# Optimization experiments

Hardware: AMD Instinct MI355X
Metric: run time of the kernel (lower is better)

## Reference

```python
import jax, jax.numpy as jnp
import numpy as np

B, C, T = 8, 256, 2048
K = 10                     # n_neigh_seq
TEMPORAL_SCALE = 2048
SHORT_RATIO = 0.4
STITCH_GAP = 20


def setup_inputs() -> dict:
    key = jax.random.key(0)
    k1, k2, k3, k4 = jax.random.split(key, 4)
    x = jax.random.normal(k1, (B, C, T), dtype=jnp.float32)
    num_frms = jax.random.randint(k2, (B,), 0, 2048, dtype=jnp.int64 if jax.config.jax_enable_x64 else jnp.int32)
    W_conv = jax.random.normal(k3, (C, C, 3), dtype=jnp.float32) * 0.02  # Conv1d(out,in,k)
    b_conv = jnp.zeros((C,), dtype=jnp.float32)
    W_mlp = jax.random.normal(k4, (C, 2 * C), dtype=jnp.float32) * 0.02  # Linear(2C -> C)
    b_mlp = jnp.zeros((C,), dtype=jnp.float32)
    return {"x": x, "num_frms": num_frms, "W_conv": W_conv, "b_conv": b_conv,
            "W_mlp": W_mlp, "b_mlp": b_mlp}


def knn_neigh_idx(x, num_frms, k=K):
    """Vectorized translation of knn() + get_neigh_idx_semantic()."""
    b, c, t = x.shape
    ratio = TEMPORAL_SCALE / t
    half1 = k // 2
    half2 = k - half1
    # pairwise squared distances via ||xi||^2 + ||xj||^2 - 2 xi.xj (same math,
    # avoids the B*C*T*T intermediate the torch code materializes)
    sq = jnp.sum(x * x, axis=1)                           # [B,T]
    gram = jnp.einsum('bci,bcj->bij', x, x)               # [B,T,T]
    dif = sq[:, :, None] + sq[:, None, :] - 2.0 * gram    # [B,T,T]
    _, idx_org = jax.lax.top_k(-dif, k)                   # smallest-k -> [B,T,k]
    big = jnp.max(dif) + 1.0
    # per-batch short-video rewiring (original does a python loop over batch)
    cond = num_frms.astype(jnp.float32) <= SHORT_RATIO * TEMPORAL_SCALE   # [B]
    thr = (num_frms.astype(jnp.float32) + STITCH_GAP) / ratio             # [B]
    pos = jnp.arange(t)
    region = (pos[None, :, None] >= thr[:, None, None]) & \
             (pos[None, None, :] >= thr[:, None, None])                   # [B,T,T]
    dif_m = jnp.where(region, big, dif)
    # kill the already-chosen first half of neighbors, then re-topk the rest
    b_idx = jnp.arange(b)[:, None, None]
    r_idx = pos[None, :, None]
    dif_m = dif_m.at[b_idx, r_idx, idx_org[:, :, :half1]].set(big)
    _, idx2 = jax.lax.top_k(-dif_m, half2)                # [B,T,half2]
    tail = jnp.where(cond[:, None, None], idx2, idx_org[:, :, half1:])
    idx_new = jnp.concatenate([idx_org[:, :, :half1], tail], axis=-1)     # [B,T,k]
    shift = (jnp.arange(b) * t)[:, None, None]
    return (idx_new + shift).reshape(-1)                  # [B*T*k] flat node ids


def reference(x, num_frms, W_conv, b_conv, W_mlp, b_mlp):
    b, c, t = x.shape
    # tconv1: Conv1d k=3, s=1, p=1
    c_out = jax.lax.conv_general_dilated(
        x, W_conv, window_strides=(1,), padding=[(1, 1)],
        dimension_numbers=('NCH', 'OIH', 'NCH')) + b_conv[None, :, None]   # [B,C,T]
    # NeighConv on raw x (gcn_insert == 'par'), nfeat_mode='feat_ctr', agg='max'
    neigh = knn_neigh_idx(x, num_frms)                    # [B*T*K]
    feat = jnp.transpose(x, (0, 2, 1)).reshape(-1, c)     # [B*T, C]
    feat_neigh = feat[neigh].reshape(-1, K, c)            # [B*T, K, C]
    ctr = jnp.broadcast_to(feat[:, None, :], feat_neigh.shape)
    cat = jnp.concatenate([feat_neigh, ctr], axis=-1)     # [B*T, K, 2C]
    g = jnp.einsum('nkd,od->nko', cat, W_mlp) + b_mlp     # [B*T, K, C]
    g = jnp.max(g, axis=1)                                # max aggregation
    g_out = jnp.transpose(g.reshape(b, t, -1), (0, 2, 1)) # [B,C,T]
    out = jax.nn.relu(c_out + g_out)
    # MaxPool1d(kernel=2, stride=2)
    out = out.reshape(b, out.shape[1], t // 2, 2).max(axis=-1)
    return out
```

## Files before the change

### kernel.cpp

```cpp
#include <hip/hip_runtime.h>
#include <hip/hip_bf16.h>
#include <math.h>
#include <float.h>

#define NC 256
#define NT 2048

typedef __attribute__((ext_vector_type(4))) float f32x4;
typedef __attribute__((ext_vector_type(8))) short short8;
typedef __attribute__((ext_vector_type(8))) unsigned short ushort8;

#define SQ_OFF 0
#define A_OFF  131072
#define XL_OFF 8388608
#define E_OFF  16908288
#define NB_OFF 33685504

__device__ __forceinline__ int load_nf(const int* __restrict__ nf, int b) {
    bool is64 = (nf[1] == 0) & (nf[3] == 0) & (nf[5] == 0) & (nf[7] == 0);
    return is64 ? nf[2 * b] : nf[b];
}

__device__ __forceinline__ void split_bf16(float f, unsigned short& h, unsigned short& l) {
    __hip_bfloat16 hb = __float2bfloat16(f);
    float fh = __bfloat162float(hb);
    __hip_bfloat16 lb = __float2bfloat16(f - fh);
    h = *(unsigned short*)&hb;
    l = *(unsigned short*)&lb;
}

__device__ __forceinline__ float rl_f(float v, int srclane) {
    return __int_as_float(__builtin_amdgcn_readlane(__float_as_int(v), srclane));
}
__device__ __forceinline__ int rl_i(int v, int srclane) {
    return __builtin_amdgcn_readlane(v, srclane);
}
__device__ __forceinline__ float dpp_shr1_f(float v) {
    return __int_as_float(__builtin_amdgcn_update_dpp(0, __float_as_int(v), 0x111, 0xf, 0xf, false));
}
__device__ __forceinline__ int dpp_shr1_i(int v) {
    return __builtin_amdgcn_update_dpp(0, v, 0x111, 0xf, 0xf, false);
}

__global__ __launch_bounds__(256) void k_sq(const float* __restrict__ x, double* __restrict__ sq,
                                            unsigned short* __restrict__ Xh8,
                                            unsigned short* __restrict__ Xl8) {
    __shared__ double part[8][33];
    int b = blockIdx.y;
    int q0 = blockIdx.x * 32;
    int tid = threadIdx.x;
    int tt = tid & 31, cg = tid >> 5;
    const float* xp = x + (size_t)b * NC * NT + q0 + tt;
    int t = q0 + tt;
    double a = 0.0;
    #pragma unroll
    for (int g = 0; g < 4; ++g) {
        ushort8 hv, lw;
        #pragma unroll
        for (int i = 0; i < 8; ++i) {
            float f = xp[(size_t)(cg * 32 + g * 8 + i) * NT];
            double v = (double)f;
            a = fma(v, v, a);
            unsigned short h, l;
            split_bf16(f, h, l);
            hv[i] = h; lw[i] = l;
        }
        size_t off = (((size_t)b * 32 + (cg * 4 + g)) * NT + t) * 8;
        *(ushort8*)(Xh8 + off) = hv;
        *(ushort8*)(Xl8 + off) = lw;
    }
    part[cg][tt] = a;
    __syncthreads();
    if (tid < 32) {
        double s = part[0][tid];
        #pragma unroll
        for (int g = 1; g < 8; ++g) s += part[g][tid];
        sq[b * NT + q0 + tid] = s;
    }
}

__global__ __launch_bounds__(256) void k_xt(const float* __restrict__ x, float* __restrict__ xT) {
    __shared__ float T[64][65];
    int t0 = blockIdx.x * 64, c0 = blockIdx.y * 64, b = blockIdx.z;
    int tid = threadIdx.x;
    int j = tid & 63, i0 = tid >> 6;
    #pragma unroll
    for (int i = 0; i < 16; ++i) {
        int c = i * 4 + i0;
        T[c][j] = x[((size_t)b * NC + c0 + c) * NT + t0 + j];
    }
    __syncthreads();
    #pragma unroll
    for (int i = 0; i < 16; ++i) {
        int t = i * 4 + i0;
        xT[((size_t)b * NT + t0 + t) * NC + c0 + j] = T[j][t];
    }
}

__global__ __launch_bounds__(256) void k_wsplit(const float* __restrict__ Wc, const float* __restrict__ Wm,
                                                unsigned short* __restrict__ wsc) {
    int o = blockIdx.x;
    int tid = threadIdx.x;
    #pragma unroll
    for (int i = 0; i < 3; ++i) {
        int idx = i * 256 + tid;
        int c = idx / 3, kh = idx % 3;
        float w = Wc[(size_t)o * 768 + idx];
        if (kh == 1) w += Wm[(size_t)o * 512 + 256 + c];
        unsigned short h, l;
        split_bf16(w, h, l);
        wsc[(size_t)(kh * 256 + o) * 256 + c] = h;
        wsc[196608 + (size_t)(kh * 256 + o) * 256 + c] = l;
    }
    float wa = Wm[(size_t)o * 512 + tid];
    unsigned short h, l;
    split_bf16(wa, h, l);
    wsc[393216 + (size_t)o * 256 + tid] = h;
    wsc[458752 + (size_t)o * 256 + tid] = l;
}

#define XQH_S 264
#define DFA_S 66

#define LD_CHUNK(chx, ph, pl) do { \
    size_t o_ = ((size_t)(((chx) & 7) * 4 + quad) * NT + (size_t)((((chx) >> 3) << 6) + n0)) * 8; \
    ph = *(const short8*)(Xh8b + o_); \
    pl = *(const short8*)(Xl8b + o_); \
  } while (0)

__global__ __launch_bounds__(256) void k_knn_a(const unsigned short* __restrict__ Xh8,
                                               const unsigned short* __restrict__ Xl8,
                                               const double* __restrict__ sq,
                                               const int* __restrict__ nf,
                                               unsigned short* __restrict__ cand,
                                               unsigned short* __restrict__ cand2) {
    __shared__ __align__(16) unsigned short Qh[16 * XQH_S];
    __shared__ __align__(16) unsigned short Ql[16 * XQH_S];
    __shared__ __align__(16) float Df[16 * DFA_S];
    int q0 = blockIdx.x * 16;
    int b = blockIdx.y;
    int tid = threadIdx.x;
    int lane = tid & 63, wave = tid >> 6;
    const unsigned short* Xh8b = Xh8 + (size_t)b * 32 * NT * 8;
    const unsigned short* Xl8b = Xl8 + (size_t)b * 32 * NT * 8;
    const double* sqb = sq + b * NT;
    int n = load_nf(nf, b);
    int thr = n + 20;
    bool need2 = (n <= 819) && (q0 + 15 >= thr);
    float lv[4], lv2[4];
    int li[4], li2[4];
    #pragma unroll
    for (int rr = 0; rr < 4; ++rr) { lv[rr] = INFINITY; li[rr] = 0; lv2[rr] = INFINITY; li2[rr] = 0; }
    #pragma unroll
    for (int i = 0; i < 2; ++i) {
        int idx = tid + i * 256;
        int q = idx & 15, cgp = idx >> 4;
        size_t off = (((size_t)cgp) * NT + q0 + q) * 8;
        uint4 vh = *(const uint4*)(Xh8b + off);
        uint4 vl = *(const uint4*)(Xl8b + off);
        *(uint4*)&Qh[q * XQH_S + cgp * 8] = vh;
        *(uint4*)&Ql[q * XQH_S + cgp * 8] = vl;
    }
    int quad = lane >> 4, l15 = lane & 15;
    int qrow = l15;
    int n0 = wave * 16 + l15;
    float sqv[4];
    #pragma unroll
    for (int bb = 0; bb < 4; ++bb) sqv[bb] = (float)sqb[q0 + quad * 4 + bb];
    __syncthreads();
    const int nch = (NT / 64) * 8;
    short8 hA[4], lA[4];
    LD_CHUNK(0, hA[0], lA[0]);
    LD_CHUNK(1, hA[1], lA[1]);
    LD_CHUNK(2, hA[2], lA[2]);
    LD_CHUNK(3, hA[3], lA[3]);
    int ch = 0;
    for (int k0 = 0; k0 < NT; k0 += 64) {
        f32x4 acc0 = {0.f, 0.f, 0.f, 0.f};
        float sk0 = (float)sqb[k0 + n0];
        #pragma unroll
        for (int cc = 0; cc < 8; ++cc) {
            const int bi = cc & 3;
            short8 bh = hA[bi], bl = lA[bi];
            int chn = ch + 4;
            if (chn > nch - 1) chn = nch - 1;
            LD_CHUNK(chn, hA[bi], lA[bi]);
            int cb = cc << 5;
            short8 ah = *(const short8*)&Qh[qrow * XQH_S + cb + quad * 8];
            short8 al = *(const short8*)&Ql[qrow * XQH_S + cb + quad * 8];
            acc0 = __builtin_amdgcn_mfma_f32_16x16x32_bf16(al, bh, acc0, 0, 0, 0);
            acc0 = __builtin_amdgcn_mfma_f32_16x16x32_bf16(ah, bl, acc0, 0, 0, 0);
            acc0 = __builtin_amdgcn_mfma_f32_16x16x32_bf16(ah, bh, acc0, 0, 0, 0);
            ++ch;
        }
        #pragma unroll
        for (int bb = 0; bb < 4; ++bb) {
            int mr = quad * 4 + bb;
            Df[mr * DFA_S + n0] = sqv[bb] + sk0 - 2.f * acc0[bb];
        }
        __syncthreads();
        bool do2 = need2 && (k0 < thr);
        unsigned long long vmask = do2 ? __ballot((k0 + lane) < thr) : 0ull;
        float dnext = Df[(wave * 4) * DFA_S + lane];
        #pragma unroll
        for (int rr = 0; rr < 4; ++rr) {
            float d = dnext;
            if (rr < 3) dnext = Df[(wave * 4 + rr + 1) * DFA_S + lane];
            {
                float thr16 = rl_f(lv[rr], 15);
                unsigned long long mask = __ballot(d < thr16);
                while (mask) {
                    int bit = __ffsll(mask) - 1;
                    mask &= mask - 1;
                    float vv = rl_f(d, bit);
                    int jj = k0 + bit;
                    unsigned long long le = __ballot(lv[rr] <= vv);
                    int pos = __popcll(le);
                    float pv = dpp_shr1_f(lv[rr]);
                    int pj = dpp_shr1_i(li[rr]);
                    if (lane < 16) {
                        if (lane == pos)      { lv[rr] = vv; li[rr] = jj; }
                        else if (lane > pos)  { lv[rr] = pv; li[rr] = pj; }
                    }
                    mask &= __ballot(d < rl_f(lv[rr], 15));
                }
            }
            if (do2) {
                float thr24 = rl_f(lv2[rr], 23);
                unsigned long long mask = __ballot(d < thr24) & vmask;
                while (mask) {
                    int bit = __ffsll(mask) - 1;
                    mask &= mask - 1;
                    float vv = rl_f(d, bit);
                    int jj = k0 + bit;
                    unsigned long long le = __ballot(lv2[rr] <= vv);
                    int pos = __popcll(le);
                    float pv = dpp_shr1_f(lv2[rr]);
                    int pj = dpp_shr1_i(li2[rr]);
                    if (lane == 16) { pv = rl_f(lv2[rr], 15); pj = rl_i(li2[rr], 15); }
                    if (lane < 24) {
                        if (lane == pos)      { lv2[rr] = vv; li2[rr] = jj; }
                        else if (lane > pos)  { lv2[rr] = pv; li2[rr] = pj; }
                    }
                    mask &= __ballot(d < rl_f(lv2[rr], 23));
                }
            }
        }
        __syncthreads();
    }
    if (lane < 16) {
        #pragma unroll
        for (int rr = 0; rr < 4; ++rr)
            cand[((size_t)b * NT + q0 + wave * 4 + rr) * 16 + lane] = (unsigned short)li[rr];
    }
    if (need2 && lane < 24) {
        #pragma unroll
        for (int rr = 0; rr < 4; ++rr) {
            unsigned short v = (lv2[rr] == INFINITY) ? 0xFFFFu : (unsigned short)li2[rr];
            cand2[((size_t)b * NT + q0 + wave * 4 + rr) * 24 + lane] = v;
        }
    }
}

__global__ __launch_bounds__(256) void k_rr1(const float* __restrict__ xT, const double* __restrict__ sq,
                                             const unsigned short* __restrict__ cand, int* __restrict__ nb) {
    int b = blockIdx.y;
    int wave = threadIdx.x >> 6, lane = threadIdx.x & 63;
    int t = blockIdx.x * 4 + wave;
    const float* qp = &xT[((size_t)b * NT + t) * NC];
    float4 q4 = *(const float4*)&qp[lane * 4];
    const unsigned short* cr = &cand[((size_t)b * NT + t) * 16];
    double sqt = sq[b * NT + t];
    double myd = 0.0; int myc = 0;
    for (int i = 0; i < 16; ++i) {
        int t2 = cr[i];
        float4 k4 = *(const float4*)&xT[((size_t)b * NT + t2) * NC + lane * 4];
        double s = fma((double)q4.w, (double)k4.w,
                   fma((double)q4.z, (double)k4.z,
                   fma((double)q4.y, (double)k4.y, (double)q4.x * (double)k4.x)));
        #pragma unroll
        for (int off = 32; off; off >>= 1) s += __shfl_xor(s, off);
        double d = sqt + sq[b * NT + t2] - 2.0 * s;
        if (lane == i) { myd = d; myc = t2; }
    }
    int rank = 0;
    for (int j = 0; j < 16; ++j) {
        double dj = __shfl(myd, j);
        int cj = __shfl(myc, j);
        if (lane < 16 && j != lane)
            rank += ((dj < myd) || (dj == myd && cj < myc)) ? 1 : 0;
    }
    if (lane < 16 && rank < 10) nb[((size_t)b * NT + t) * 10 + rank] = myc;
}

__global__ __launch_bounds__(256) void k_rr2(const float* __restrict__ xT, const double* __restrict__ sq,
                                             const int* __restrict__ nf,
                                             const unsigned short* __restrict__ cand2,
                                             int* __restrict__ nb) {
    int b = blockIdx.y;
    int n = load_nf(nf, b);
    if (n > 819) return;
    int thr = n + 20;
    int wave = threadIdx.x >> 6, lane = threadIdx.x & 63;
    int t = blockIdx.x * 4 + wave;
    if (blockIdx.x * 4 + 3 < thr) return;
    bool active = (t >= thr);
    const float* qp = &xT[((size_t)b * NT + t) * NC];
    float4 q4 = *(const float4*)&qp[lane * 4];
    const unsigned short* cr = &cand2[((size_t)b * NT + t) * 24];
    double sqt = sq[b * NT + t];
    double myd = DBL_MAX; int myc = 0x7FFFFFFF;
    for (int i = 0; i < 24; ++i) {
        int c16 = cr[i];
        if (c16 == 0xFFFF) continue;
        int t2 = c16;
        float4 k4 = *(const float4*)&xT[((size_t)b * NT + t2) * NC + lane * 4];
        double s = fma((double)q4.w, (double)k4.w,
                   fma((double)q4.z, (double)k4.z,
                   fma((double)q4.y, (double)k4.y, (double)q4.x * (double)k4.x)));
        #pragma unroll
        for (int off = 32; off; off >>= 1) s += __shfl_xor(s, off);
        double d = sqt + sq[b * NT + t2] - 2.0 * s;
        if (lane == i) { myd = d; myc = t2; }
    }
    if (!active) return;
    int f[5];
    #pragma unroll
    for (int s = 0; s < 5; ++s) f[s] = nb[((size_t)b * NT + t) * 10 + s];
    bool keep = (lane < 24) && (myc != 0x7FFFFFFF);
    #pragma unroll
    for (int s = 0; s < 5; ++s) keep = keep && (myc != f[s]);
    int rank = 0;
    for (int j = 0; j < 24; ++j) {
        double dj = __shfl(myd, j);
        int cj = __shfl(myc, j);
        bool kj = __shfl((int)keep, j);
        if (keep && kj && j != lane)
            rank += ((dj < myd) || (dj == myd && cj < myc)) ? 1 : 0;
    }
    if (keep && rank < 5) nb[((size_t)b * NT + t) * 10 + 5 + rank] = myc;
}

#define XT_S 40

__global__ __launch_bounds__(256) void k_conv(const float* __restrict__ x, const unsigned short* __restrict__ wsc,
                                              const float* __restrict__ bc, const float* __restrict__ bm,
                                              float* __restrict__ E, float* __restrict__ A) {
    __shared__ __align__(16) unsigned short XTh[66 * XT_S], XTl[66 * XT_S];
    __shared__ __align__(16) unsigned short Wsh[3 * 64 * XT_S], Wsl[3 * 64 * XT_S];
    __shared__ __align__(16) unsigned short Wah[64 * XT_S], Wal[64 * XT_S];
    int tx = blockIdx.x * 64, oy = blockIdx.y * 64, b = blockIdx.z;
    int tid = threadIdx.x, lane = tid & 63, wave = tid >> 6;
    int quad = lane >> 4, l15 = lane & 15;
    f32x4 accE[4] = {}, accA[4] = {};
    for (int c0 = 0; c0 < 256; c0 += 32) {
        __syncthreads();
        #pragma unroll
        for (int i = 0; i < 8; ++i) {
            int c = wave * 8 + i;
            int t = lane;
            int g = tx - 1 + t;
            float v = (g >= 0 && g < NT) ? x[((size_t)b * NC + c0 + c) * NT + g] : 0.f;
            unsigned short h, l;
            split_bf16(v, h, l);
            XTh[t * XT_S + c] = h;
            XTl[t * XT_S + c] = l;
        }
        if (tid < 64) {
            int c = tid >> 1, t = 64 + (tid & 1);
            int g = tx - 1 + t;
            float v = (g < NT) ? x[((size_t)b * NC + c0 + c) * NT + g] : 0.f;
            unsigned short h, l;
            split_bf16(v, h, l);
            XTh[t * XT_S + c] = h;
            XTl[t * XT_S + c] = l;
        }
        #pragma unroll
        for (int i = 0; i < 3; ++i) {
            int gidx = i * 256 + tid;
            int kh = gidx >> 8;
            int o  = (gidx >> 2) & 63;
            int g4 = gidx & 3;
            uint4 vh = *(const uint4*)&wsc[(size_t)(kh * 256 + oy + o) * 256 + c0 + g4 * 8];
            *(uint4*)&Wsh[(kh * 64 + o) * XT_S + g4 * 8] = vh;
            uint4 vl = *(const uint4*)&wsc[196608 + (size_t)(kh * 256 + oy + o) * 256 + c0 + g4 * 8];
            *(uint4*)&Wsl[(kh * 64 + o) * XT_S + g4 * 8] = vl;
        }
        {
            int o = tid >> 2, g4 = tid & 3;
            uint4 vh = *(const uint4*)&wsc[393216 + (size_t)(oy + o) * 256 + c0 + g4 * 8];
            *(uint4*)&Wah[o * XT_S + g4 * 8] = vh;
            uint4 vl = *(const uint4*)&wsc[458752 + (size_t)(oy + o) * 256 + c0 + g4 * 8];
            *(uint4*)&Wal[o * XT_S + g4 * 8] = vl;
        }
        __syncthreads();
        int trow = wave * 16 + l15;
        short8 a_h[3], a_l[3];
        #pragma unroll
        for (int kh = 0; kh < 3; ++kh) {
            a_h[kh] = *(const short8*)&XTh[(trow + kh) * XT_S + quad * 8];
            a_l[kh] = *(const short8*)&XTl[(trow + kh) * XT_S + quad * 8];
        }
        #pragma unroll
        for (int ns = 0; ns < 4; ++ns) {
            int orow = ns * 16 + l15;
            short8 wa_h = *(const short8*)&Wah[orow * XT_S + quad * 8];
            short8 wa_l = *(const short8*)&Wal[orow * XT_S + quad * 8];
            accA[ns] = __builtin_amdgcn_mfma_f32_16x16x32_bf16(a_l[1], wa_h, accA[ns], 0, 0, 0);
            accA[ns] = __builtin_amdgcn_mfma_f32_16x16x32_bf16(a_h[1], wa_l, accA[ns], 0, 0, 0);
            accA[ns] = __builtin_amdgcn_mfma_f32_16x16x32_bf16(a_h[1], wa_h, accA[ns], 0, 0, 0);
            #pragma unroll
            for (int kh = 0; kh < 3; ++kh) {
                short8 w_h = *(const short8*)&Wsh[(kh * 64 + orow) * XT_S + quad * 8];
                short8 w_l = *(const short8*)&Wsl[(kh * 64 + orow) * XT_S + quad * 8];
                accE[ns] = __builtin_amdgcn_mfma_f32_16x16x32_bf16(a_l[kh], w_h, accE[ns], 0, 0, 0);
                accE[ns] = __builtin_amdgcn_mfma_f32_16x16x32_bf16(a_h[kh], w_l, accE[ns], 0, 0, 0);
                accE[ns] = __builtin_amdgcn_mfma_f32_16x16x32_bf16(a_h[kh], w_h, accE[ns], 0, 0, 0);
            }
        }
    }
    #pragma unroll
    for (int ns = 0; ns < 4; ++ns) {
        int o = oy + ns * 16 + l15;
        float bias = bc[o] + bm[o];
        #pragma unroll
        for (int r = 0; r < 4; ++r) {
            int t = tx + wave * 16 + quad * 4 + r;
            E[((size_t)b * NT + t) * 256 + o] = accE[ns][r] + bias;
            A[((size_t)b * NT + t) * 256 + o] = accA[ns][r];
        }
    }
}

__global__ __launch_bounds__(256) void k_epi(const float* __restrict__ A, const float* __restrict__ E,
                                             const int* __restrict__ nb, float* __restrict__ out) {
    __shared__ float buf[32 * 260];
    int p0 = blockIdx.x * 32;
    int b = blockIdx.y;
    int tid = threadIdx.x;
    int o4 = tid & 63;
    int pg = tid >> 6;
    for (int pp8 = 0; pp8 < 8; ++pp8) {
        int pp = pg * 8 + pp8;
        int p = p0 + pp;
        float vm[4] = {0.f, 0.f, 0.f, 0.f};
        #pragma unroll
        for (int tt = 0; tt < 2; ++tt) {
            int t = p * 2 + tt;
            const int* nrow = &nb[((size_t)b * NT + t) * 10];
            float gm[4] = {-FLT_MAX, -FLT_MAX, -FLT_MAX, -FLT_MAX};
            #pragma unroll
            for (int k = 0; k < 10; ++k) {
                int t2 = nrow[k] & (NT - 1);
                float4 a = *(const float4*)&A[((size_t)b * NT + t2) * 256 + o4 * 4];
                gm[0] = fmaxf(gm[0], a.x); gm[1] = fmaxf(gm[1], a.y);
                gm[2] = fmaxf(gm[2], a.z); gm[3] = fmaxf(gm[3], a.w);
            }
            float4 e = *(const float4*)&E[((size_t)b * NT + t) * 256 + o4 * 4];
            vm[0] = fmaxf(vm[0], fmaxf(e.x + gm[0], 0.f));
            vm[1] = fmaxf(vm[1], fmaxf(e.y + gm[1], 0.f));
            vm[2] = fmaxf(vm[2], fmaxf(e.z + gm[2], 0.f));
            vm[3] = fmaxf(vm[3], fmaxf(e.w + gm[3], 0.f));
        }
        float4 v = {vm[0], vm[1], vm[2], vm[3]};
        *(float4*)&buf[pp * 260 + o4 * 4] = v;
    }
    __syncthreads();
    #pragma unroll
    for (int i = 0; i < 32; ++i) {
        int idx = tid + i * 256;
        int oo = idx >> 5, pp = idx & 31;
        out[((size_t)b * 256 + oo) * 1024 + p0 + pp] = buf[pp * 260 + oo];
    }
}

extern "C" void kernel_launch(void* const* d_in, const int* in_sizes, int n_in,
                              void* d_out, int out_size, void* d_ws, size_t ws_size,
                              hipStream_t stream) {
    const float* x  = (const float*)d_in[0];
    const int*   nf = (const int*)d_in[1];
    const float* Wc = (const float*)d_in[2];
    const float* bc = (const float*)d_in[3];
    const float* Wm = (const float*)d_in[4];
    const float* bm = (const float*)d_in[5];
    float* out = (float*)d_out;
    char* ws = (char*)d_ws;
    double* sq = (double*)(ws + SQ_OFF);
    float* A   = (float*)(ws + A_OFF);
    float* E   = (float*)(ws + E_OFF);
    int* nb    = (int*)(ws + NB_OFF);
    unsigned short* Xh8 = (unsigned short*)(ws + A_OFF);
    unsigned short* Xl8 = (unsigned short*)(ws + A_OFF + XL_OFF);
    float* xT = (float*)(ws + E_OFF);
    unsigned short* wsc   = (unsigned short*)d_out;
    unsigned short* cand  = (unsigned short*)d_out + (1 << 20);
    unsigned short* cand2 = (unsigned short*)d_out + (1 << 20) + (1 << 19);

    k_sq<<<dim3(64, 8), dim3(256), 0, stream>>>(x, sq, Xh8, Xl8);
    k_xt<<<dim3(32, 4, 8), dim3(256), 0, stream>>>(x, xT);
    k_wsplit<<<dim3(256), dim3(256), 0, stream>>>(Wc, Wm, wsc);
    k_knn_a<<<dim3(128, 8), dim3(256), 0, stream>>>(Xh8, Xl8, sq, nf, cand, cand2);
    k_rr1<<<dim3(512, 8), dim3(256), 0, stream>>>(xT, sq, cand, nb);
    k_rr2<<<dim3(512, 8), dim3(256), 0, stream>>>(xT, sq, nf, cand2, nb);
    k_conv<<<dim3(32, 4, 8), dim3(256), 0, stream>>>(x, wsc, bc, bm, E, A);
    k_epi<<<dim3(32, 8), dim3(256), 0, stream>>>(A, E, nb, out);
}
```

Baseline: 477.8 us.

## Split KNN key range across two blocks and fuse transpose into sq kernel

The KNN candidate kernel now splits the key dimension into two halves on a new grid axis. Each half emits its own 16 candidates, so each query row gets 32 candidates, and the rerank kernel now ranks all 32. This doubles the number of blocks to improve GPU fill, at the cost of extra exact-distance rerank work. The secondary (short-video) candidate search stays on the first half only, since every valid key there lies below the threshold. The separate transpose kernel is folded into the squared-norm/bf16-split kernel through an LDS tile, saving one launch and one extra read of x.

```diff
diff --git a/kernel.cpp b/kernel.cpp
--- a/kernel.cpp
+++ b/kernel.cpp
@@ -42,9 +42,11 @@
     return __builtin_amdgcn_update_dpp(0, v, 0x111, 0xf, 0xf, false);
 }
 
-__global__ __launch_bounds__(256) void k_sq(const float* __restrict__ x, double* __restrict__ sq,
-                                            unsigned short* __restrict__ Xh8,
-                                            unsigned short* __restrict__ Xl8) {
+__global__ __launch_bounds__(256) void k_sqt(const float* __restrict__ x, double* __restrict__ sq,
+                                             unsigned short* __restrict__ Xh8,
+                                             unsigned short* __restrict__ Xl8,
+                                             float* __restrict__ xT) {
+    __shared__ float Txc[32][257];
     __shared__ double part[8][33];
     int b = blockIdx.y;
     int q0 = blockIdx.x * 32;
@@ -58,12 +60,14 @@
         ushort8 hv, lw;
         #pragma unroll
         for (int i = 0; i < 8; ++i) {
-            float f = xp[(size_t)(cg * 32 + g * 8 + i) * NT];
+            int c = cg * 32 + g * 8 + i;
+            float f = xp[(size_t)c * NT];
             double v = (double)f;
             a = fma(v, v, a);
             unsigned short h, l;
             split_bf16(f, h, l);
             hv[i] = h; lw[i] = l;
+            Txc[tt][c] = f;
         }
         size_t off = (((size_t)b * 32 + (cg * 4 + g)) * NT + t) * 8;
         *(ushort8*)(Xh8 + off) = hv;
@@ -77,24 +81,9 @@
         for (int g = 1; g < 8; ++g) s += part[g][tid];
         sq[b * NT + q0 + tid] = s;
     }
-}
-
-__global__ __launch_bounds__(256) void k_xt(const float* __restrict__ x, float* __restrict__ xT) {
-    __shared__ float T[64][65];
-    int t0 = blockIdx.x * 64, c0 = blockIdx.y * 64, b = blockIdx.z;
-    int tid = threadIdx.x;
-    int j = tid & 63, i0 = tid >> 6;
-    #pragma unroll
-    for (int i = 0; i < 16; ++i) {
-        int c = i * 4 + i0;
-        T[c][j] = x[((size_t)b * NC + c0 + c) * NT + t0 + j];
-    }
-    __syncthreads();
-    #pragma unroll
-    for (int i = 0; i < 16; ++i) {
-        int t = i * 4 + i0;
-        xT[((size_t)b * NT + t0 + t) * NC + c0 + j] = T[j][t];
-    }
+    #pragma unroll 8
+    for (int r = 0; r < 32; ++r)
+        xT[((size_t)b * NT + q0 + r) * NC + tid] = Txc[r][tid];
 }
 
 __global__ __launch_bounds__(256) void k_wsplit(const float* __restrict__ Wc, const float* __restrict__ Wm,
@@ -138,7 +127,8 @@
     __shared__ __align__(16) unsigned short Ql[16 * XQH_S];
     __shared__ __align__(16) float Df[16 * DFA_S];
     int q0 = blockIdx.x * 16;
-    int b = blockIdx.y;
+    int h = blockIdx.y;
+    int b = blockIdx.z;
     int tid = threadIdx.x;
     int lane = tid & 63, wave = tid >> 6;
     const unsigned short* Xh8b = Xh8 + (size_t)b * 32 * NT * 8;
@@ -146,7 +136,7 @@
     const double* sqb = sq + b * NT;
     int n = load_nf(nf, b);
     int thr = n + 20;
-    bool need2 = (n <= 819) && (q0 + 15 >= thr);
+    bool need2 = (h == 0) && (n <= 819) && (q0 + 15 >= thr);
     float lv[4], lv2[4];
     int li[4], li2[4];
     #pragma unroll
@@ -168,14 +158,15 @@
     #pragma unroll
     for (int bb = 0; bb < 4; ++bb) sqv[bb] = (float)sqb[q0 + quad * 4 + bb];
     __syncthreads();
-    const int nch = (NT / 64) * 8;
+    const int k_begin = h * 1024, k_end = k_begin + 1024;
+    const int ch_last = (h + 1) * 128 - 1;
     short8 hA[4], lA[4];
-    LD_CHUNK(0, hA[0], lA[0]);
-    LD_CHUNK(1, hA[1], lA[1]);
-    LD_CHUNK(2, hA[2], lA[2]);
-    LD_CHUNK(3, hA[3], lA[3]);
-    int ch = 0;
-    for (int k0 = 0; k0 < NT; k0 += 64) {
+    int ch = h * 128;
+    LD_CHUNK(ch + 0, hA[0], lA[0]);
+    LD_CHUNK(ch + 1, hA[1], lA[1]);
+    LD_CHUNK(ch + 2, hA[2], lA[2]);
+    LD_CHUNK(ch + 3, hA[3], lA[3]);
+    for (int k0 = k_begin; k0 < k_end; k0 += 64) {
         f32x4 acc0 = {0.f, 0.f, 0.f, 0.f};
         float sk0 = (float)sqb[k0 + n0];
         #pragma unroll
@@ -183,7 +174,7 @@
             const int bi = cc & 3;
             short8 bh = hA[bi], bl = lA[bi];
             int chn = ch + 4;
-            if (chn > nch - 1) chn = nch - 1;
+            if (chn > ch_last) chn = ch_last;
             LD_CHUNK(chn, hA[bi], lA[bi]);
             int cb = cc << 5;
             short8 ah = *(const short8*)&Qh[qrow * XQH_S + cb + quad * 8];
@@ -251,7 +242,7 @@
     if (lane < 16) {
         #pragma unroll
         for (int rr = 0; rr < 4; ++rr)
-            cand[((size_t)b * NT + q0 + wave * 4 + rr) * 16 + lane] = (unsigned short)li[rr];
+            cand[((size_t)b * NT + q0 + wave * 4 + rr) * 32 + h * 16 + lane] = (unsigned short)li[rr];
     }
     if (need2 && lane < 24) {
         #pragma unroll
@@ -269,10 +260,10 @@
     int t = blockIdx.x * 4 + wave;
     const float* qp = &xT[((size_t)b * NT + t) * NC];
     float4 q4 = *(const float4*)&qp[lane * 4];
-    const unsigned short* cr = &cand[((size_t)b * NT + t) * 16];
+    const unsigned short* cr = &cand[((size_t)b * NT + t) * 32];
     double sqt = sq[b * NT + t];
-    double myd = 0.0; int myc = 0;
-    for (int i = 0; i < 16; ++i) {
+    double myd = DBL_MAX; int myc = 0x7FFFFFFF;
+    for (int i = 0; i < 32; ++i) {
         int t2 = cr[i];
         float4 k4 = *(const float4*)&xT[((size_t)b * NT + t2) * NC + lane * 4];
         double s = fma((double)q4.w, (double)k4.w,
@@ -284,13 +275,13 @@
         if (lane == i) { myd = d; myc = t2; }
     }
     int rank = 0;
-    for (int j = 0; j < 16; ++j) {
+    for (int j = 0; j < 32; ++j) {
         double dj = __shfl(myd, j);
         int cj = __shfl(myc, j);
-        if (lane < 16 && j != lane)
+        if (lane < 32 && j != lane)
             rank += ((dj < myd) || (dj == myd && cj < myc)) ? 1 : 0;
     }
-    if (lane < 16 && rank < 10) nb[((size_t)b * NT + t) * 10 + rank] = myc;
+    if (lane < 32 && rank < 10) nb[((size_t)b * NT + t) * 10 + rank] = myc;
 }
 
 __global__ __launch_bounds__(256) void k_rr2(const float* __restrict__ xT, const double* __restrict__ sq,
@@ -496,10 +487,9 @@
     unsigned short* cand  = (unsigned short*)d_out + (1 << 20);
     unsigned short* cand2 = (unsigned short*)d_out + (1 << 20) + (1 << 19);
 
-    k_sq<<<dim3(64, 8), dim3(256), 0, stream>>>(x, sq, Xh8, Xl8);
-    k_xt<<<dim3(32, 4, 8), dim3(256), 0, stream>>>(x, xT);
+    k_sqt<<<dim3(64, 8), dim3(256), 0, stream>>>(x, sq, Xh8, Xl8, xT);
     k_wsplit<<<dim3(256), dim3(256), 0, stream>>>(Wc, Wm, wsc);
-    k_knn_a<<<dim3(128, 8), dim3(256), 0, stream>>>(Xh8, Xl8, sq, nf, cand, cand2);
+    k_knn_a<<<dim3(128, 2, 8), dim3(256), 0, stream>>>(Xh8, Xl8, sq, nf, cand, cand2);
     k_rr1<<<dim3(512, 8), dim3(256), 0, stream>>>(xT, sq, cand, nb);
     k_rr2<<<dim3(512, 8), dim3(256), 0, stream>>>(xT, sq, nf, cand2, nb);
     k_conv<<<dim3(32, 4, 8), dim3(256), 0, stream>>>(x, wsc, bc, bm, E, A);
```

Result: slower. 559.6 us (+17.1%).
